# Optimization experiments

Measured on AMD Instinct MI355X. Metric: run time of the kernel, lower is better.

The kernel has to match this reference:

```python
import jax, jax.numpy as jnp
import numpy as np

H, DH, DM = 8, 128, 1024          # n_head, d_head, d_model (n_head*d_head == d_model)
SLEN, BSZ = 256, 64               # slen <= 256 forced by pi0[:, :l]
SCALE = 1.0 / DH ** 0.5
LN_EPS = 1e-5


def setup_inputs() -> dict:
    key = jax.random.key(0)
    k0, k1, k2, k3 = jax.random.split(key, 4)
    h = jax.random.normal(k0, (SLEN, BSZ, DM), jnp.float32)
    W_qkv = jax.random.normal(k1, (H * 4 * DH, DM), jnp.float32) * (DM ** -0.5)
    W_o = jax.random.normal(k2, (DM, H * DH), jnp.float32) * ((H * DH) ** -0.5)
    pi0 = jax.random.uniform(k3, (H, 256), jnp.float32)
    ln_gamma = jnp.ones((DM,), jnp.float32)
    ln_beta = jnp.zeros((DM,), jnp.float32)
    return {"h": h, "W_qkv": W_qkv, "W_o": W_o, "pi0": pi0,
            "ln_gamma": ln_gamma, "ln_beta": ln_beta}


def _phi(x):
    # elu(x)+1 feature map, then L1-normalize over the feature dim
    x = jax.nn.elu(x) + 1.0
    return x / jnp.sum(x, axis=-1, keepdims=True)


def _causal_linear_attn(q, k, v):
    # fast_weight_sum: out_t = sum_{s<=t} (q_t . k_s) v_s  (zero initial fast weights)
    # q,k,v: [b,h,l,d]
    l = q.shape[2]
    scores = jnp.einsum('bhld,bhsd->bhls', q, k)
    mask = jnp.tril(jnp.ones((l, l), dtype=bool))
    scores = jnp.where(mask, scores, jnp.zeros((), scores.dtype))
    return jnp.einsum('bhls,bhsd->bhld', scores, v)


def reference(h, W_qkv, W_o, pi0, ln_gamma, ln_beta):
    l, b, _ = h.shape
    # qkv projection: [l,b,H,4*DH] -> q, k1, k2, v (update_mode='rbf2keys')
    qkv = jnp.einsum('lbm,nm->lbn', h, W_qkv).reshape(l, b, H, 4 * DH)
    q, k1, k2, v = jnp.split(qkv, 4, axis=-1)
    # permute to [b, H, l, d]
    q = _phi(jnp.transpose(q, (1, 2, 0, 3)))
    k1 = _phi(jnp.transpose(k1, (1, 2, 0, 3)))
    k2 = _phi(jnp.transpose(k2, (1, 2, 0, 3)))
    v = jnp.transpose(v, (1, 2, 0, 3))
    # two fast-weight sums (skip_attn_normalization=True path)
    lo1 = _causal_linear_attn(q, k1, v)
    lo2 = _causal_linear_attn(q, k2, v)
    pi = jnp.clip(pi0, 0.0, 1.0)[None, :, :l, None]          # [1,H,l,1]
    layer_out = SCALE * (lo1 * pi + lo2 * (1.0 - pi))         # [b,H,l,d]
    # [b,H,l,d] -> [l,b,H*d]
    layer_out = jnp.transpose(layer_out, (2, 0, 1, 3)).reshape(l, b, H * DH)
    attn_out = jnp.einsum('lbn,mn->lbm', layer_out, W_o)
    # post-LN residual (pre_lnorm=False, dropout=0)
    x = h + attn_out
    mu = jnp.mean(x, axis=-1, keepdims=True)
    var = jnp.mean((x - mu) ** 2, axis=-1, keepdims=True)
    return ln_gamma * (x - mu) / jnp.sqrt(var + LN_EPS) + ln_beta
```

## Files before the change

### kernel.cpp

```cpp
#include <hip/hip_runtime.h>

#define H_     8
#define DM_    1024
#define NQKV_  4096
#define ROWS_  16384
#define PAIRS_ 512
#define SCALE_ 0.08838834764831845f
#define LN_EPS_ 1e-5f

typedef __attribute__((ext_vector_type(8))) short short8;
typedef __attribute__((ext_vector_type(4))) float floatx4;

__device__ __forceinline__ float b2f(unsigned short u) {
  union { unsigned int i; float f; } v; v.i = ((unsigned int)u) << 16; return v.f;
}
__device__ __forceinline__ unsigned short f2b(float f) {
  union { unsigned int i; float f; } v; v.f = f;
  unsigned int b = v.i;
  b += 0x7FFFu + ((b >> 16) & 1u);
  return (unsigned short)(b >> 16);
}

__device__ __forceinline__ void stage_async(const unsigned short* __restrict__ g,
                                            size_t ld, unsigned short* s, int tid) {
#pragma unroll
  for (int p = 0; p < 4; ++p) {
    int idx = p * 256 + tid;
    int r = idx >> 3, j = idx & 7;
    int cg = j ^ (r & 7);
    __builtin_amdgcn_global_load_lds(
        (const __attribute__((address_space(1))) unsigned int*)(g + (size_t)r * ld + cg * 8),
        (__attribute__((address_space(3))) unsigned int*)(s + (size_t)idx * 8),
        16, 0, 0);
  }
}
__device__ __forceinline__ short8 lds_frag(const unsigned short* s, int row, int cg) {
  return *(const short8*)(s + row * 64 + ((cg ^ (row & 7)) << 3));
}

__global__ __launch_bounds__(256) void cvt_all(const float* __restrict__ h,
                                               const float* __restrict__ wq,
                                               const float* __restrict__ wo,
                                               unsigned short* __restrict__ hb,
                                               unsigned short* __restrict__ wqb,
                                               unsigned short* __restrict__ wob) {
  int i = blockIdx.x * 256 + threadIdx.x;
  const float* src; unsigned short* dst; int off;
  if (i < 2097152)      { src = h;  dst = hb;  off = i; }
  else if (i < 2621440) { src = wq; dst = wqb; off = i - 2097152; }
  else                  { src = wo; dst = wob; off = i - 2621440; }
  const float4* s4 = (const float4*)(src + (size_t)off * 8);
  float4 v0 = s4[0], v1 = s4[1];
  union { short8 v; unsigned short u[8]; } pk;
  pk.u[0] = f2b(v0.x); pk.u[1] = f2b(v0.y); pk.u[2] = f2b(v0.z); pk.u[3] = f2b(v0.w);
  pk.u[4] = f2b(v1.x); pk.u[5] = f2b(v1.y); pk.u[6] = f2b(v1.z); pk.u[7] = f2b(v1.w);
  *(short8*)(dst + (size_t)off * 8) = pk.v;
}

__global__ __launch_bounds__(256, 4) void qkv_gemm(const unsigned short* __restrict__ A,
                                                   const unsigned short* __restrict__ B,
                                                   unsigned short* __restrict__ QKV) {
  __shared__ alignas(16) unsigned short Sh[17408];
  unsigned short* As = Sh;
  unsigned short* Bs = Sh + 8192;
  int tid = threadIdx.x;
  int lane = tid & 63, wid = tid >> 6;
  int wm = wid >> 1, wn = wid & 1;
  int quad = lane >> 4, l16 = lane & 15;
  int m0 = blockIdx.y * 128, n0 = blockIdx.x * 128;
  int hh = n0 >> 9, part = (n0 >> 7) & 3;
  int bb = blockIdx.y & 63, lhalf = blockIdx.y >> 6;

  const unsigned short* Ab;
  size_t lda;
  if (part == 3) { Ab = A + ((size_t)(lhalf * 128) * 64 + bb) * DM_; lda = (size_t)64 * DM_; }
  else           { Ab = A + (size_t)m0 * DM_;                        lda = DM_; }
  const unsigned short* Bb = B + (size_t)n0 * DM_;

  floatx4 acc[4][4];
#pragma unroll
  for (int i = 0; i < 4; ++i)
#pragma unroll
    for (int j = 0; j < 4; ++j)
#pragma unroll
      for (int r = 0; r < 4; ++r) acc[i][j][r] = 0.f;

  for (int kt = 0; kt < DM_; kt += 64) {
    stage_async(Ab + kt, lda, As, tid);
    stage_async(Bb + kt, DM_, Bs, tid);
    __syncthreads();
#pragma unroll
    for (int kk = 0; kk < 2; ++kk) {
      short8 af[4], bfv[4];
#pragma unroll
      for (int mt = 0; mt < 4; ++mt)
        af[mt] = lds_frag(As, wm * 64 + mt * 16 + l16, kk * 4 + quad);
#pragma unroll
      for (int nt = 0; nt < 4; ++nt)
        bfv[nt] = lds_frag(Bs, wn * 64 + nt * 16 + l16, kk * 4 + quad);
#pragma unroll
      for (int mt = 0; mt < 4; ++mt)
#pragma unroll
        for (int nt = 0; nt < 4; ++nt)
          acc[mt][nt] = __builtin_amdgcn_mfma_f32_16x16x32_bf16(af[mt], bfv[nt], acc[mt][nt], 0, 0, 0);
    }
    __syncthreads();
  }

  if (part < 3) {
    unsigned short* P = QKV + (size_t)part * 16777216;
    float rsum[4][4];
#pragma unroll
    for (int mt = 0; mt < 4; ++mt)
#pragma unroll
      for (int r = 0; r < 4; ++r) rsum[mt][r] = 0.f;
#pragma unroll
    for (int mt = 0; mt < 4; ++mt)
#pragma unroll
      for (int nt = 0; nt < 4; ++nt)
#pragma unroll
        for (int r = 0; r < 4; ++r) {
          float x = acc[mt][nt][r];
          float f = x > 0.f ? x + 1.f : __expf(x);
          acc[mt][nt][r] = f;
          rsum[mt][r] += f;
        }
#pragma unroll
    for (int off = 1; off < 16; off <<= 1)
#pragma unroll
      for (int mt = 0; mt < 4; ++mt)
#pragma unroll
        for (int r = 0; r < 4; ++r)
          rsum[mt][r] += __shfl_xor(rsum[mt][r], off);
    float* red = (float*)Sh;
    if (l16 == 0) {
#pragma unroll
      for (int mt = 0; mt < 4; ++mt)
#pragma unroll
        for (int r = 0; r < 4; ++r)
          red[wn * 128 + wm * 64 + mt * 16 + quad * 4 + r] = rsum[mt][r];
    }
    __syncthreads();
#pragma unroll
    for (int mt = 0; mt < 4; ++mt)
#pragma unroll
      for (int r = 0; r < 4; ++r) {
        int rl = wm * 64 + mt * 16 + quad * 4 + r;
        float inv = 1.f / (red[rl] + red[128 + rl]);
        int row = m0 + rl;
        int l = row >> 6, b = row & 63;
        size_t base = ((size_t)((b * 8 + hh) * 256 + l)) * 128;
#pragma unroll
        for (int nt = 0; nt < 4; ++nt) {
          int d = wn * 64 + nt * 16 + l16;
          P[base + d] = f2b(acc[mt][nt][r] * inv);
        }
      }
  } else {
    unsigned short* T = Sh;
#pragma unroll
    for (int mt = 0; mt < 4; ++mt)
#pragma unroll
      for (int nt = 0; nt < 4; ++nt)
#pragma unroll
        for (int r = 0; r < 4; ++r) {
          int l = wm * 64 + mt * 16 + quad * 4 + r;
          int d = wn * 64 + nt * 16 + l16;
          T[d * 136 + l] = f2b(acc[mt][nt][r]);
        }
    __syncthreads();
    unsigned short* Vt = QKV + (size_t)3 * 16777216;
    int d = tid >> 1, lb = (tid & 1) * 64;
    size_t gbase = ((size_t)((bb * 8 + hh) * 128 + d)) * 256 + lhalf * 128 + lb;
    const unsigned short* trow = T + d * 136 + lb;
#pragma unroll
    for (int j = 0; j < 8; ++j)
      *(short8*)(Vt + gbase + j * 8) = *(const short8*)(trow + j * 8);
  }
}

__global__ __launch_bounds__(256) void scores_kernel(const unsigned short* __restrict__ QKV,
                                                     const float* __restrict__ pi0,
                                                     unsigned short* __restrict__ S) {
  __shared__ alignas(16) unsigned short As[128 * 64], Bs1[128 * 64], Bs2[128 * 64];
  __shared__ float pis[128];
  int p = blockIdx.z;
  int hh = p & 7;
  int tid = threadIdx.x;
  int lane = tid & 63, wid = tid >> 6;
  int wm = wid >> 1, wn = wid & 1;
  int quad = lane >> 4, l16 = lane & 15;
  int tix = blockIdx.x;
  int m0 = (tix >= 1) ? 128 : 0;
  int n0 = (tix == 2) ? 128 : 0;
  if (tid < 128) {
    float pv = pi0[hh * 256 + m0 + tid];
    pis[tid] = fminf(fmaxf(pv, 0.f), 1.f);
  }
  const unsigned short* Qb  = QKV + (size_t)p * 32768 + (size_t)m0 * 128;
  const unsigned short* K1b = QKV + 16777216     + (size_t)p * 32768 + (size_t)n0 * 128;
  const unsigned short* K2b = QKV + 2 * 16777216 + (size_t)p * 32768 + (size_t)n0 * 128;

  floatx4 acc1[4][4], acc2[4][4];
#pragma unroll
  for (int i = 0; i < 4; ++i)
#pragma unroll
    for (int j = 0; j < 4; ++j)
#pragma unroll
      for (int r = 0; r < 4; ++r) { acc1[i][j][r] = 0.f; acc2[i][j][r] = 0.f; }

  for (int kt = 0; kt < 128; kt += 64) {
    stage_async(Qb + kt, 128, As, tid);
    stage_async(K1b + kt, 128, Bs1, tid);
    stage_async(K2b + kt, 128, Bs2, tid);
    __syncthreads();
#pragma unroll
    for (int kk = 0; kk < 2; ++kk) {
      short8 af[4], b1[4], b2v[4];
#pragma unroll
      for (int mt = 0; mt < 4; ++mt)
        af[mt] = lds_frag(As, wm * 64 + mt * 16 + l16, kk * 4 + quad);
#pragma unroll
      for (int nt = 0; nt < 4; ++nt) {
        b1[nt]  = lds_frag(Bs1, wn * 64 + nt * 16 + l16, kk * 4 + quad);
        b2v[nt] = lds_frag(Bs2, wn * 64 + nt * 16 + l16, kk * 4 + quad);
      }
#pragma unroll
      for (int mt = 0; mt < 4; ++mt)
#pragma unroll
        for (int nt = 0; nt < 4; ++nt) {
          acc1[mt][nt] = __builtin_amdgcn_mfma_f32_16x16x32_bf16(af[mt], b1[nt],  acc1[mt][nt], 0, 0, 0);
          acc2[mt][nt] = __builtin_amdgcn_mfma_f32_16x16x32_bf16(af[mt], b2v[nt], acc2[mt][nt], 0, 0, 0);
        }
    }
    __syncthreads();
  }
#pragma unroll
  for (int mt = 0; mt < 4; ++mt)
#pragma unroll
    for (int nt = 0; nt < 4; ++nt)
#pragma unroll
      for (int r = 0; r < 4; ++r) {
        int tl = wm * 64 + mt * 16 + quad * 4 + r;
        int t = m0 + tl;
        int s = n0 + wn * 64 + nt * 16 + l16;
        float pv = pis[tl];
        float v = (s <= t) ? (pv * acc1[mt][nt][r] + (1.f - pv) * acc2[mt][nt][r]) : 0.f;
        S[(size_t)p * 65536 + (size_t)t * 256 + s] = f2b(v);
      }
}

__global__ __launch_bounds__(256, 4) void pv_kernel(const unsigned short* __restrict__ S,
                                                    const unsigned short* __restrict__ Vt,
                                                    unsigned short* __restrict__ LO) {
  __shared__ alignas(16) unsigned short As[128 * 64], Bs[128 * 64];
  int p = blockIdx.z;
  int b = p >> 3, hh = p & 7;
  int tid = threadIdx.x;
  int lane = tid & 63, wid = tid >> 6;
  int wm = wid >> 1, wn = wid & 1;
  int quad = lane >> 4, l16 = lane & 15;
  int m0 = blockIdx.y * 128;
  int kEnd = (blockIdx.y == 0) ? 128 : 256;
  const unsigned short* Ab = S  + (size_t)p * 65536 + (size_t)m0 * 256;
  const unsigned short* Bb = Vt + (size_t)p * 32768;

  floatx4 acc[4][4];
#pragma unroll
  for (int i = 0; i < 4; ++i)
#pragma unroll
    for (int j = 0; j < 4; ++j)
#pragma unroll
      for (int r = 0; r < 4; ++r) acc[i][j][r] = 0.f;

  for (int kt = 0; kt < kEnd; kt += 64) {
    stage_async(Ab + kt, 256, As, tid);
    stage_async(Bb + kt, 256, Bs, tid);
    __syncthreads();
#pragma unroll
    for (int kk = 0; kk < 2; ++kk) {
      short8 af[4], bfv[4];
#pragma unroll
      for (int mt = 0; mt < 4; ++mt)
        af[mt] = lds_frag(As, wm * 64 + mt * 16 + l16, kk * 4 + quad);
#pragma unroll
      for (int nt = 0; nt < 4; ++nt)
        bfv[nt] = lds_frag(Bs, wn * 64 + nt * 16 + l16, kk * 4 + quad);
#pragma unroll
      for (int mt = 0; mt < 4; ++mt)
#pragma unroll
        for (int nt = 0; nt < 4; ++nt)
          acc[mt][nt] = __builtin_amdgcn_mfma_f32_16x16x32_bf16(af[mt], bfv[nt], acc[mt][nt], 0, 0, 0);
    }
    __syncthreads();
  }
#pragma unroll
  for (int mt = 0; mt < 4; ++mt)
#pragma unroll
    for (int nt = 0; nt < 4; ++nt)
#pragma unroll
      for (int r = 0; r < 4; ++r) {
        int t = m0 + wm * 64 + mt * 16 + quad * 4 + r;
        int dcol = wn * 64 + nt * 16 + l16;
        LO[((size_t)t * 64 + b) * 1024 + hh * 128 + dcol] = f2b(SCALE_ * acc[mt][nt][r]);
      }
}

__global__ __launch_bounds__(256, 4) void wo_gemm(const unsigned short* __restrict__ A,
                                                  const unsigned short* __restrict__ B,
                                                  const float* __restrict__ hin,
                                                  float* __restrict__ X) {
  __shared__ alignas(16) unsigned short As[128 * 64], Bs[128 * 64];
  int tid = threadIdx.x;
  int lane = tid & 63, wid = tid >> 6;
  int wm = wid >> 1, wn = wid & 1;
  int quad = lane >> 4, l16 = lane & 15;
  int m0 = blockIdx.y * 128, n0 = blockIdx.x * 128;
  const unsigned short* Ab = A + (size_t)m0 * DM_;
  const unsigned short* Bb = B + (size_t)n0 * DM_;

  floatx4 acc[4][4];
#pragma unroll
  for (int i = 0; i < 4; ++i)
#pragma unroll
    for (int j = 0; j < 4; ++j)
#pragma unroll
      for (int r = 0; r < 4; ++r) acc[i][j][r] = 0.f;

  for (int kt = 0; kt < DM_; kt += 64) {
    stage_async(Ab + kt, DM_, As, tid);
    stage_async(Bb + kt, DM_, Bs, tid);
    __syncthreads();
#pragma unroll
    for (int kk = 0; kk < 2; ++kk) {
      short8 af[4], bfv[4];
#pragma unroll
      for (int mt = 0; mt < 4; ++mt)
        af[mt] = lds_frag(As, wm * 64 + mt * 16 + l16, kk * 4 + quad);
#pragma unroll
      for (int nt = 0; nt < 4; ++nt)
        bfv[nt] = lds_frag(Bs, wn * 64 + nt * 16 + l16, kk * 4 + quad);
#pragma unroll
      for (int mt = 0; mt < 4; ++mt)
#pragma unroll
        for (int nt = 0; nt < 4; ++nt)
          acc[mt][nt] = __builtin_amdgcn_mfma_f32_16x16x32_bf16(af[mt], bfv[nt], acc[mt][nt], 0, 0, 0);
    }
    __syncthreads();
  }
#pragma unroll
  for (int mt = 0; mt < 4; ++mt)
#pragma unroll
    for (int nt = 0; nt < 4; ++nt)
#pragma unroll
      for (int r = 0; r < 4; ++r) {
        int row = m0 + wm * 64 + mt * 16 + quad * 4 + r;
        int col = n0 + wn * 64 + nt * 16 + l16;
        size_t idx = (size_t)row * DM_ + col;
        X[idx] = acc[mt][nt][r] + hin[idx];
      }
}

__global__ __launch_bounds__(256) void ln_kernel(float* __restrict__ X,
                                                 const float* __restrict__ gamma,
                                                 const float* __restrict__ beta) {
  int row = blockIdx.x;
  int tid = threadIdx.x;
  float* x = X + (size_t)row * DM_;
  float4 v = *(const float4*)(x + tid * 4);
  float s  = v.x + v.y + v.z + v.w;
  float ss = v.x * v.x + v.y * v.y + v.z * v.z + v.w * v.w;
#pragma unroll
  for (int off = 32; off; off >>= 1) {
    s  += __shfl_down(s, off);
    ss += __shfl_down(ss, off);
  }
  __shared__ float rs[4], rss[4];
  int wv = tid >> 6, lane = tid & 63;
  if (lane == 0) { rs[wv] = s; rss[wv] = ss; }
  __syncthreads();
  float St  = rs[0] + rs[1] + rs[2] + rs[3];
  float SSt = rss[0] + rss[1] + rss[2] + rss[3];
  float mu = St * (1.f / DM_);
  float var = SSt * (1.f / DM_) - mu * mu;
  float rstd = rsqrtf(var + LN_EPS_);
  float4 o;
#pragma unroll
  for (int j = 0; j < 4; ++j) {
    int c = tid * 4 + j;
    (&o.x)[j] = gamma[c] * ((&v.x)[j] - mu) * rstd + beta[c];
  }
  *(float4*)(x + tid * 4) = o;
}

extern "C" void kernel_launch(void* const* d_in, const int* in_sizes, int n_in,
                              void* d_out, int out_size, void* d_ws, size_t ws_size,
                              hipStream_t stream) {
  const float* h     = (const float*)d_in[0];
  const float* Wqkv  = (const float*)d_in[1];
  const float* Wo    = (const float*)d_in[2];
  const float* pi0   = (const float*)d_in[3];
  const float* gamma = (const float*)d_in[4];
  const float* beta  = (const float*)d_in[5];
  char* ws = (char*)d_ws;

  unsigned short* QKV   = (unsigned short*)ws;
  unsigned short* Sbuf  = (unsigned short*)(ws + 134217728ull);
  unsigned short* hb    = (unsigned short*)(ws + 134217728ull);
  unsigned short* Wqkvb = (unsigned short*)(ws + 134217728ull + 33554432ull);
  unsigned short* Wob   = (unsigned short*)(ws + 201326592ull);
  unsigned short* LO    = (unsigned short*)ws;
  float* X = (float*)d_out;

  dim3 blk(256);
  cvt_all<<<dim3(10752), blk, 0, stream>>>(h, Wqkv, Wo, hb, Wqkvb, Wob);
  qkv_gemm<<<dim3(NQKV_ / 128, ROWS_ / 128, 1), blk, 0, stream>>>(hb, Wqkvb, QKV);
  scores_kernel<<<dim3(3, 1, PAIRS_), blk, 0, stream>>>(QKV, pi0, Sbuf);
  pv_kernel<<<dim3(1, 2, PAIRS_), blk, 0, stream>>>(Sbuf, QKV + (size_t)3 * 16777216, LO);
  wo_gemm<<<dim3(DM_ / 128, ROWS_ / 128, 1), blk, 0, stream>>>(LO, Wob, h, X);
  ln_kernel<<<dim3(ROWS_, 1, 1), blk, 0, stream>>>(X, gamma, beta);
}
```

Before: 494.3 us.

## Fuse scores and PV kernels into one flash-style attention kernel

Merges the scores and PV kernels into a single attention kernel. Each block computes a 128x128 score tile for both key sets, mixes them with pi, applies the causal mask, keeps the tile in LDS with an XOR swizzle, and multiplies it by V straight away. This removes the global round trip of the bf16 score matrix and one kernel launch. It also routes the qkv_gemm epilogue's normalized output stores through LDS so that global writes become coalesced 16-byte rows. The cost is a grid of 1024 blocks with uneven work (block 1 handles two score chunks), higher LDS use at 2 blocks per CU, and Q being restaged for each chunk.

Result: slower. 621.2 us (+25.7%).

```diff
diff --git a/kernel.cpp b/kernel.cpp
--- a/kernel.cpp
+++ b/kernel.cpp
@@ -141,21 +141,34 @@
           red[wn * 128 + wm * 64 + mt * 16 + quad * 4 + r] = rsum[mt][r];
     }
     __syncthreads();
+    float inv[4][4];
 #pragma unroll
     for (int mt = 0; mt < 4; ++mt)
 #pragma unroll
       for (int r = 0; r < 4; ++r) {
         int rl = wm * 64 + mt * 16 + quad * 4 + r;
-        float inv = 1.f / (red[rl] + red[128 + rl]);
-        int row = m0 + rl;
-        int l = row >> 6, b = row & 63;
-        size_t base = ((size_t)((b * 8 + hh) * 256 + l)) * 128;
-#pragma unroll
-        for (int nt = 0; nt < 4; ++nt) {
+        inv[mt][r] = 1.f / (red[rl] + red[128 + rl]);
+      }
+    __syncthreads();
+#pragma unroll
+    for (int mt = 0; mt < 4; ++mt)
+#pragma unroll
+      for (int nt = 0; nt < 4; ++nt)
+#pragma unroll
+        for (int r = 0; r < 4; ++r) {
+          int rl = wm * 64 + mt * 16 + quad * 4 + r;
           int d = wn * 64 + nt * 16 + l16;
-          P[base + d] = f2b(acc[mt][nt][r] * inv);
+          Sh[rl * 136 + d] = f2b(acc[mt][nt][r] * inv[mt][r]);
         }
-      }
+    __syncthreads();
+    int row = tid >> 1, halfc = tid & 1;
+    int grow = m0 + row;
+    int l = grow >> 6, bidx = grow & 63;
+    size_t gbase = ((size_t)((bidx * 8 + hh) * 256 + l)) * 128 + halfc * 64;
+    const unsigned short* trow = Sh + row * 136 + halfc * 64;
+#pragma unroll
+    for (int j = 0; j < 8; ++j)
+      *(short8*)(P + gbase + j * 8) = *(const short8*)(trow + j * 8);
   } else {
     unsigned short* T = Sh;
 #pragma unroll
@@ -179,120 +192,105 @@
   }
 }
 
-__global__ __launch_bounds__(256) void scores_kernel(const unsigned short* __restrict__ QKV,
-                                                     const float* __restrict__ pi0,
-                                                     unsigned short* __restrict__ S) {
-  __shared__ alignas(16) unsigned short As[128 * 64], Bs1[128 * 64], Bs2[128 * 64];
-  __shared__ float pis[128];
-  int p = blockIdx.z;
-  int hh = p & 7;
+__global__ __launch_bounds__(256, 2) void attn_kernel(const unsigned short* __restrict__ QKV,
+                                                      const float* __restrict__ pi0,
+                                                      unsigned short* __restrict__ LO) {
+  __shared__ alignas(16) unsigned short Qs[8192], K1s[8192], K2s[8192], Scs[2][8192];
+  int ty = blockIdx.x;
+  int p  = blockIdx.y;
+  int b = p >> 3, hh = p & 7;
+  int t0 = ty * 128;
   int tid = threadIdx.x;
   int lane = tid & 63, wid = tid >> 6;
   int wm = wid >> 1, wn = wid & 1;
   int quad = lane >> 4, l16 = lane & 15;
-  int tix = blockIdx.x;
-  int m0 = (tix >= 1) ? 128 : 0;
-  int n0 = (tix == 2) ? 128 : 0;
-  if (tid < 128) {
-    float pv = pi0[hh * 256 + m0 + tid];
-    pis[tid] = fminf(fmaxf(pv, 0.f), 1.f);
-  }
-  const unsigned short* Qb  = QKV + (size_t)p * 32768 + (size_t)m0 * 128;
-  const unsigned short* K1b = QKV + 16777216     + (size_t)p * 32768 + (size_t)n0 * 128;
-  const unsigned short* K2b = QKV + 2 * 16777216 + (size_t)p * 32768 + (size_t)n0 * 128;
-
-  floatx4 acc1[4][4], acc2[4][4];
+
+  const unsigned short* Qb  = QKV + (size_t)p * 32768 + (size_t)t0 * 128;
+  const unsigned short* K1g = QKV + 16777216     + (size_t)p * 32768;
+  const unsigned short* K2g = QKV + 2 * 16777216 + (size_t)p * 32768;
+  const unsigned short* Vg  = QKV + (size_t)3 * 16777216 + (size_t)p * 32768;
+
+  floatx4 oacc[4][4];
 #pragma unroll
   for (int i = 0; i < 4; ++i)
 #pragma unroll
     for (int j = 0; j < 4; ++j)
 #pragma unroll
-      for (int r = 0; r < 4; ++r) { acc1[i][j][r] = 0.f; acc2[i][j][r] = 0.f; }
-
-  for (int kt = 0; kt < 128; kt += 64) {
-    stage_async(Qb + kt, 128, As, tid);
-    stage_async(K1b + kt, 128, Bs1, tid);
-    stage_async(K2b + kt, 128, Bs2, tid);
-    __syncthreads();
-#pragma unroll
-    for (int kk = 0; kk < 2; ++kk) {
-      short8 af[4], b1[4], b2v[4];
-#pragma unroll
-      for (int mt = 0; mt < 4; ++mt)
-        af[mt] = lds_frag(As, wm * 64 + mt * 16 + l16, kk * 4 + quad);
-#pragma unroll
-      for (int nt = 0; nt < 4; ++nt) {
-        b1[nt]  = lds_frag(Bs1, wn * 64 + nt * 16 + l16, kk * 4 + quad);
-        b2v[nt] = lds_frag(Bs2, wn * 64 + nt * 16 + l16, kk * 4 + quad);
-      }
-#pragma unroll
-      for (int mt = 0; mt < 4; ++mt)
+      for (int r = 0; r < 4; ++r) oacc[i][j][r] = 0.f;
+
+  for (int sc = 0; sc <= ty; ++sc) {
+    floatx4 acc1[4][4], acc2[4][4];
+#pragma unroll
+    for (int i = 0; i < 4; ++i)
+#pragma unroll
+      for (int j = 0; j < 4; ++j)
+#pragma unroll
+        for (int r = 0; r < 4; ++r) { acc1[i][j][r] = 0.f; acc2[i][j][r] = 0.f; }
+
+    for (int kt = 0; kt < 128; kt += 64) {
+      stage_async(Qb + kt, 128, Qs, tid);
+      stage_async(K1g + (size_t)sc * 16384 + kt, 128, K1s, tid);
+      stage_async(K2g + (size_t)sc * 16384 + kt, 128, K2s, tid);
+      __syncthreads();
+#pragma unroll
+      for (int kk = 0; kk < 2; ++kk) {
+        short8 af[4], b1[4], b2v[4];
+#pragma unroll
+        for (int mt = 0; mt < 4; ++mt)
+          af[mt] = lds_frag(Qs, wm * 64 + mt * 16 + l16, kk * 4 + quad);
 #pragma unroll
         for (int nt = 0; nt < 4; ++nt) {
-          acc1[mt][nt] = __builtin_amdgcn_mfma_f32_16x16x32_bf16(af[mt], b1[nt],  acc1[mt][nt], 0, 0, 0);
-          acc2[mt][nt] = __builtin_amdgcn_mfma_f32_16x16x32_bf16(af[mt], b2v[nt], acc2[mt][nt], 0, 0, 0);
+          b1[nt]  = lds_frag(K1s, wn * 64 + nt * 16 + l16, kk * 4 + quad);
+          b2v[nt] = lds_frag(K2s, wn * 64 + nt * 16 + l16, kk * 4 + quad);
         }
+#pragma unroll
+        for (int mt = 0; mt < 4; ++mt)
+#pragma unroll
+          for (int nt = 0; nt < 4; ++nt) {
+            acc1[mt][nt] = __builtin_amdgcn_mfma_f32_16x16x32_bf16(af[mt], b1[nt],  acc1[mt][nt], 0, 0, 0);
+            acc2[mt][nt] = __builtin_amdgcn_mfma_f32_16x16x32_bf16(af[mt], b2v[nt], acc2[mt][nt], 0, 0, 0);
+          }
+      }
+      __syncthreads();
     }
-    __syncthreads();
-  }
-#pragma unroll
-  for (int mt = 0; mt < 4; ++mt)
-#pragma unroll
-    for (int nt = 0; nt < 4; ++nt)
+#pragma unroll
+    for (int mt = 0; mt < 4; ++mt)
 #pragma unroll
       for (int r = 0; r < 4; ++r) {
         int tl = wm * 64 + mt * 16 + quad * 4 + r;
-        int t = m0 + tl;
-        int s = n0 + wn * 64 + nt * 16 + l16;
-        float pv = pis[tl];
-        float v = (s <= t) ? (pv * acc1[mt][nt][r] + (1.f - pv) * acc2[mt][nt][r]) : 0.f;
-        S[(size_t)p * 65536 + (size_t)t * 256 + s] = f2b(v);
-      }
-}
-
-__global__ __launch_bounds__(256, 4) void pv_kernel(const unsigned short* __restrict__ S,
-                                                    const unsigned short* __restrict__ Vt,
-                                                    unsigned short* __restrict__ LO) {
-  __shared__ alignas(16) unsigned short As[128 * 64], Bs[128 * 64];
-  int p = blockIdx.z;
-  int b = p >> 3, hh = p & 7;
-  int tid = threadIdx.x;
-  int lane = tid & 63, wid = tid >> 6;
-  int wm = wid >> 1, wn = wid & 1;
-  int quad = lane >> 4, l16 = lane & 15;
-  int m0 = blockIdx.y * 128;
-  int kEnd = (blockIdx.y == 0) ? 128 : 256;
-  const unsigned short* Ab = S  + (size_t)p * 65536 + (size_t)m0 * 256;
-  const unsigned short* Bb = Vt + (size_t)p * 32768;
-
-  floatx4 acc[4][4];
-#pragma unroll
-  for (int i = 0; i < 4; ++i)
-#pragma unroll
-    for (int j = 0; j < 4; ++j)
-#pragma unroll
-      for (int r = 0; r < 4; ++r) acc[i][j][r] = 0.f;
-
-  for (int kt = 0; kt < kEnd; kt += 64) {
-    stage_async(Ab + kt, 256, As, tid);
-    stage_async(Bb + kt, 256, Bs, tid);
-    __syncthreads();
-#pragma unroll
-    for (int kk = 0; kk < 2; ++kk) {
-      short8 af[4], bfv[4];
-#pragma unroll
-      for (int mt = 0; mt < 4; ++mt)
-        af[mt] = lds_frag(As, wm * 64 + mt * 16 + l16, kk * 4 + quad);
-#pragma unroll
-      for (int nt = 0; nt < 4; ++nt)
-        bfv[nt] = lds_frag(Bs, wn * 64 + nt * 16 + l16, kk * 4 + quad);
-#pragma unroll
-      for (int mt = 0; mt < 4; ++mt)
+        float pv = pi0[hh * 256 + t0 + tl];
+        pv = fminf(fmaxf(pv, 0.f), 1.f);
+#pragma unroll
+        for (int nt = 0; nt < 4; ++nt) {
+          int sl = wn * 64 + nt * 16 + l16;
+          float v = pv * acc1[mt][nt][r] + (1.f - pv) * acc2[mt][nt][r];
+          if (sc == ty && sl > tl) v = 0.f;
+          int col = sl & 63, half = sl >> 6;
+          Scs[half][tl * 64 + ((((col >> 3) ^ (tl & 7))) << 3) + (col & 7)] = f2b(v);
+        }
+      }
+    __syncthreads();
+#pragma unroll
+    for (int kc = 0; kc < 2; ++kc) {
+      stage_async(Vg + sc * 128 + kc * 64, 256, K1s, tid);
+      __syncthreads();
+#pragma unroll
+      for (int kk = 0; kk < 2; ++kk) {
+        short8 af[4], bfv[4];
+#pragma unroll
+        for (int mt = 0; mt < 4; ++mt)
+          af[mt] = lds_frag(Scs[kc], wm * 64 + mt * 16 + l16, kk * 4 + quad);
 #pragma unroll
         for (int nt = 0; nt < 4; ++nt)
-          acc[mt][nt] = __builtin_amdgcn_mfma_f32_16x16x32_bf16(af[mt], bfv[nt], acc[mt][nt], 0, 0, 0);
+          bfv[nt] = lds_frag(K1s, wn * 64 + nt * 16 + l16, kk * 4 + quad);
+#pragma unroll
+        for (int mt = 0; mt < 4; ++mt)
+#pragma unroll
+          for (int nt = 0; nt < 4; ++nt)
+            oacc[mt][nt] = __builtin_amdgcn_mfma_f32_16x16x32_bf16(af[mt], bfv[nt], oacc[mt][nt], 0, 0, 0);
+      }
+      __syncthreads();
     }
-    __syncthreads();
   }
 #pragma unroll
   for (int mt = 0; mt < 4; ++mt)
@@ -300,9 +298,9 @@
     for (int nt = 0; nt < 4; ++nt)
 #pragma unroll
       for (int r = 0; r < 4; ++r) {
-        int t = m0 + wm * 64 + mt * 16 + quad * 4 + r;
-        int dcol = wn * 64 + nt * 16 + l16;
-        LO[((size_t)t * 64 + b) * 1024 + hh * 128 + dcol] = f2b(SCALE_ * acc[mt][nt][r]);
+        int t = t0 + wm * 64 + mt * 16 + quad * 4 + r;
+        int d = wn * 64 + nt * 16 + l16;
+        LO[((size_t)t * 64 + b) * 1024 + hh * 128 + d] = f2b(SCALE_ * oacc[mt][nt][r]);
       }
 }
 
@@ -405,18 +403,16 @@
   char* ws = (char*)d_ws;
 
   unsigned short* QKV   = (unsigned short*)ws;
-  unsigned short* Sbuf  = (unsigned short*)(ws + 134217728ull);
   unsigned short* hb    = (unsigned short*)(ws + 134217728ull);
-  unsigned short* Wqkvb = (unsigned short*)(ws + 134217728ull + 33554432ull);
-  unsigned short* Wob   = (unsigned short*)(ws + 201326592ull);
-  unsigned short* LO    = (unsigned short*)ws;
+  unsigned short* LO    = (unsigned short*)(ws + 134217728ull);
+  unsigned short* Wqkvb = (unsigned short*)(ws + 167772160ull);
+  unsigned short* Wob   = (unsigned short*)(ws + 176160768ull);
   float* X = (float*)d_out;
 
   dim3 blk(256);
   cvt_all<<<dim3(10752), blk, 0, stream>>>(h, Wqkv, Wo, hb, Wqkvb, Wob);
   qkv_gemm<<<dim3(NQKV_ / 128, ROWS_ / 128, 1), blk, 0, stream>>>(hb, Wqkvb, QKV);
-  scores_kernel<<<dim3(3, 1, PAIRS_), blk, 0, stream>>>(QKV, pi0, Sbuf);
-  pv_kernel<<<dim3(1, 2, PAIRS_), blk, 0, stream>>>(Sbuf, QKV + (size_t)3 * 16777216, LO);
+  attn_kernel<<<dim3(2, PAIRS_), blk, 0, stream>>>(QKV, pi0, LO);
   wo_gemm<<<dim3(DM_ / 128, ROWS_ / 128, 1), blk, 0, stream>>>(LO, Wob, h, X);
   ln_kernel<<<dim3(ROWS_, 1, 1), blk, 0, stream>>>(X, gamma, beta);
 }
```
